# Performance work log

Measured on AMD Instinct MI355X. Metric: run time of the kernel, lower is better.

Reference implementation:

```python
import jax, jax.numpy as jnp
import numpy as np

HIDDEN, NHEAD, NLAYERS = 128, 8, 4
N, H, W = 1, 36, 192


def _layernorm(x, w, b, eps=1e-5):
    mu = x.mean(-1, keepdims=True)
    var = ((x - mu) ** 2).mean(-1, keepdims=True)
    return (x - mu) * jax.lax.rsqrt(var + eps) * w + b


def _mha_rel(q_in, k_in, v_in, in_w, in_b, out_w, out_b, pos_sel, attn_mask):
    # q_in/k_in/v_in: [w, bsz, C]; pos_sel: [w, w, C] (already gathered by pos_indexes)
    w, bsz, C = q_in.shape
    hd = C // NHEAD
    scale = float(hd) ** -0.5
    wq, wk, wv = in_w[:C], in_w[C:2 * C], in_w[2 * C:]
    bq, bk, bv = in_b[:C], in_b[C:2 * C], in_b[2 * C:]
    q = (q_in @ wq.T + bq) * scale
    k = k_in @ wk.T + bk
    v = v_in @ wv.T + bv
    q_r = (pos_sel @ wq.T + bq) * scale            # [w,w,C]
    k_r = pos_sel @ wk.T + bk                       # [w,w,C]
    q = q.reshape(w, bsz, NHEAD, hd)
    k = k.reshape(w, bsz, NHEAD, hd)
    v = v.reshape(w, bsz, NHEAD, hd)
    q_r = q_r.reshape(w, w, NHEAD, hd)
    k_r = k_r.reshape(w, w, NHEAD, hd)
    # content-content + content-pos + pos-content -> [bsz, heads, w, w]
    attn = (jnp.einsum('wnec,vnec->newv', q, k)
            + jnp.einsum('wnec,wvec->newv', q, k_r)
            + jnp.einsum('vnec,wvec->newv', k, q_r))
    if attn_mask is not None:
        attn = attn + attn_mask[None, None]
    raw = attn
    a = jax.nn.softmax(attn, axis=-1)
    vo = jnp.einsum('newv,vnec->wnec', a, v).reshape(w, bsz, C)
    vo = vo @ out_w.T + out_b
    return vo, raw.sum(axis=1)  # raw summed over heads, [bsz,w,w]


def setup_inputs():
    key = jax.random.key(0)
    ks = jax.random.split(key, 8)
    C, L = HIDDEN, NLAYERS
    s = 0.02
    rn = lambda k, shape, sc: jax.random.normal(k, shape, dtype=jnp.float32) * sc
    return dict(
        feat_left=rn(ks[0], (N, C, H, W), 1.0),
        feat_right=rn(ks[1], (N, C, H, W), 1.0),
        pos_enc=rn(ks[2], (2 * W - 1, C), 1.0),
        sa_in_w=rn(ks[3], (L, 3 * C, C), s),
        sa_in_b=jnp.zeros((L, 3 * C), jnp.float32),
        sa_out_w=rn(ks[4], (L, C, C), s),
        sa_out_b=jnp.zeros((L, C), jnp.float32),
        sa_ln_w=jnp.ones((L, C), jnp.float32),
        sa_ln_b=jnp.zeros((L, C), jnp.float32),
        ca_in_w=rn(ks[5], (L, 3 * C, C), s),
        ca_in_b=jnp.zeros((L, 3 * C), jnp.float32),
        ca_out_w=rn(ks[6], (L, C, C), s),
        ca_out_b=jnp.zeros((L, C), jnp.float32),
        ca_ln1_w=jnp.ones((L, C), jnp.float32),
        ca_ln1_b=jnp.zeros((L, C), jnp.float32),
        ca_ln2_w=jnp.ones((L, C), jnp.float32),
        ca_ln2_b=jnp.zeros((L, C), jnp.float32),
    )


def reference(feat_left, feat_right, pos_enc,
              sa_in_w, sa_in_b, sa_out_w, sa_out_b, sa_ln_w, sa_ln_b,
              ca_in_w, ca_in_b, ca_out_w, ca_out_b,
              ca_ln1_w, ca_ln1_b, ca_ln2_w, ca_ln2_b):
    n, C, h, w = feat_left.shape
    hn = h * n
    # [N,C,H,W] -> [W,HN,C]
    fl = jnp.transpose(feat_left, (3, 2, 0, 1)).reshape(w, hn, C)
    fr = jnp.transpose(feat_right, (3, 2, 0, 1)).reshape(w, hn, C)
    # relative position indexes: (w-1..0) col + (0..w-1) row, flattened
    idx = (np.arange(w - 1, -1, -1)[:, None] + np.arange(w)[None, :]).reshape(-1)
    pos_sel = pos_enc[idx].reshape(w, w, C)             # for left-query attention
    pos_sel_flip = pos_enc[::-1][idx].reshape(w, w, C)  # flipped pos for right-query
    causal_mask = jnp.triu(jnp.full((w, w), -jnp.inf, dtype=jnp.float32), k=1)

    feat = jnp.concatenate([fl, fr], axis=1)  # [W, 2HN, C]
    raw_last = None
    for i in range(NLAYERS):
        # ---- self attention on concatenated tokens ----
        f2 = _layernorm(feat, sa_ln_w[i], sa_ln_b[i])
        vo, _ = _mha_rel(f2, f2, f2, sa_in_w[i], sa_in_b[i], sa_out_w[i], sa_out_b[i],
                         pos_sel, None)
        feat = feat + vo
        # ---- cross attention (shared weights for both directions) ----
        left, right = feat[:, :hn], feat[:, hn:]
        l2 = _layernorm(left, ca_ln1_w[i], ca_ln1_b[i])
        r2 = _layernorm(right, ca_ln1_w[i], ca_ln1_b[i])
        vo, _ = _mha_rel(r2, l2, l2, ca_in_w[i], ca_in_b[i], ca_out_w[i], ca_out_b[i],
                         pos_sel_flip, None)
        right = right + vo
        mask = causal_mask if i == NLAYERS - 1 else None
        r2b = _layernorm(right, ca_ln2_w[i], ca_ln2_b[i])
        vo, raw = _mha_rel(l2, r2b, r2b, ca_in_w[i], ca_in_b[i], ca_out_w[i], ca_out_b[i],
                           pos_sel, mask)
        left = left + vo
        feat = jnp.concatenate([left, right], axis=1)
        raw_last = raw
    # raw_last: [HN, W, W] -> [N, H, W, W]
    attn_weight = raw_last.reshape(h, n, w, w).transpose(1, 0, 2, 3)
    return attn_weight, feat
```

## Files before the change

### kernel.cpp

```cpp
#include <hip/hip_runtime.h>
#include <cmath>

#define W 192
#define CC 128
#define BSA 72
#define BCA 36
#define TSA (W*BSA)
#define TCA (W*BCA)
#define CH 32
#define SLD 200

__global__ __launch_bounds__(256) void pack_feat_k(const float* __restrict__ fl,
                                                   const float* __restrict__ fr,
                                                   float* __restrict__ feat) {
  __shared__ float tile[32][33];
  int b = blockIdx.z;
  const float* src = (b < BCA) ? fl : fr;
  int h = (b < BCA) ? b : b - BCA;
  int w0 = blockIdx.x * 32, c0 = blockIdx.y * 32;
  int tx = threadIdx.x & 31, ty = threadIdx.x >> 5;
#pragma unroll
  for (int rr = 0; rr < 4; ++rr) {
    int c = ty + rr * 8;
    tile[c][tx] = src[((c0 + c) * BCA + h) * W + w0 + tx];
  }
  __syncthreads();
#pragma unroll
  for (int rr = 0; rr < 4; ++rr) {
    int wl = ty + rr * 8;
    feat[(((w0 + wl) * BSA) + b) * CC + c0 + tx] = tile[tx][wl];
  }
}

template<int TM, bool LNA>
__device__ __forceinline__ void gemm_core(
    const float* __restrict__ A, int lda, int aob, int aooff,
    const float* __restrict__ lnw, const float* __restrict__ lnb,
    const float* __restrict__ Bw, int ldb,
    const float* __restrict__ bias,
    float* __restrict__ C, float* __restrict__ Cb, int ldc,
    int M, int N, int noff, int scale_abs, int accum, int ob, int ooff) {
  constexpr int MR = TM / 16;
  constexpr int AS = TM + 4;
  __shared__ float AsT[32 * AS];
  __shared__ float BsT[32 * 132];
  int tid = threadIdx.x;
  int ty = tid >> 4, tx = tid & 15;
  int t0 = blockIdx.x * TM, n0 = blockIdx.y * 128;
  int row_l = tid >> 3, qk7 = tid & 7;
  float acc[MR][8] = {};

  float4 va[TM / 32][4];
  if constexpr (LNA) {
    float4 gv[4], bvv[4];
#pragma unroll
    for (int c4 = 0; c4 < 4; ++c4) {
      gv[c4]  = *reinterpret_cast<const float4*>(lnw + c4 * 32 + qk7 * 4);
      bvv[c4] = *reinterpret_cast<const float4*>(lnb + c4 * 32 + qk7 * 4);
    }
#pragma unroll
    for (int p = 0; p < TM / 32; ++p) {
      int ar = t0 + row_l + p * 32;
      if (ar >= M) ar = M - 1;
      int sr = (ar / aob) * BSA + (ar % aob) + aooff;
      const float* arow = A + (long)sr * lda;
      float sum = 0.f, sq = 0.f;
#pragma unroll
      for (int c4 = 0; c4 < 4; ++c4) {
        va[p][c4] = *reinterpret_cast<const float4*>(arow + c4 * 32 + qk7 * 4);
        sum += va[p][c4].x + va[p][c4].y + va[p][c4].z + va[p][c4].w;
        sq += va[p][c4].x * va[p][c4].x + va[p][c4].y * va[p][c4].y
            + va[p][c4].z * va[p][c4].z + va[p][c4].w * va[p][c4].w;
      }
      sum += __shfl_xor(sum, 1); sum += __shfl_xor(sum, 2); sum += __shfl_xor(sum, 4);
      sq  += __shfl_xor(sq, 1);  sq  += __shfl_xor(sq, 2);  sq  += __shfl_xor(sq, 4);
      float mu = sum * (1.f / 128.f);
      float var = sq * (1.f / 128.f) - mu * mu;
      float rstd = 1.0f / sqrtf(var + 1e-5f);
#pragma unroll
      for (int c4 = 0; c4 < 4; ++c4) {
        va[p][c4].x = (va[p][c4].x - mu) * rstd * gv[c4].x + bvv[c4].x;
        va[p][c4].y = (va[p][c4].y - mu) * rstd * gv[c4].y + bvv[c4].y;
        va[p][c4].z = (va[p][c4].z - mu) * rstd * gv[c4].z + bvv[c4].z;
        va[p][c4].w = (va[p][c4].w - mu) * rstd * gv[c4].w + bvv[c4].w;
      }
    }
  }

  for (int kcc = 0; kcc < 4; ++kcc) {
    int kc = kcc * 32;
#pragma unroll
    for (int p = 0; p < TM / 32; ++p) {
      int row = row_l + p * 32;
      float4 av;
      if constexpr (LNA) {
        av = va[p][kcc];
      } else {
        int arow = t0 + row;
        av = make_float4(0.f, 0.f, 0.f, 0.f);
        if (arow < M) av = *reinterpret_cast<const float4*>(A + (long)arow * lda + kc + qk7 * 4);
      }
      AsT[(qk7 * 4 + 0) * AS + row] = av.x;
      AsT[(qk7 * 4 + 1) * AS + row] = av.y;
      AsT[(qk7 * 4 + 2) * AS + row] = av.z;
      AsT[(qk7 * 4 + 3) * AS + row] = av.w;
    }
#pragma unroll
    for (int p = 0; p < 4; ++p) {
      int id = tid + p * 256;
      int row = id >> 3, qk = id & 7;
      int brow = n0 + row;
      float4 bv = make_float4(0.f, 0.f, 0.f, 0.f);
      if (brow < N) bv = *reinterpret_cast<const float4*>(Bw + (long)brow * ldb + kc + qk * 4);
      BsT[(qk * 4 + 0) * 132 + row] = bv.x;
      BsT[(qk * 4 + 1) * 132 + row] = bv.y;
      BsT[(qk * 4 + 2) * 132 + row] = bv.z;
      BsT[(qk * 4 + 3) * 132 + row] = bv.w;
    }
    __syncthreads();
#pragma unroll
    for (int k = 0; k < 32; ++k) {
      float a[MR];
      if constexpr (MR == 2) {
        float2 a0 = *reinterpret_cast<const float2*>(&AsT[k * AS + ty * 2]);
        a[0] = a0.x; a[1] = a0.y;
      } else if constexpr (MR == 4) {
        float4 a0 = *reinterpret_cast<const float4*>(&AsT[k * AS + ty * 4]);
        a[0] = a0.x; a[1] = a0.y; a[2] = a0.z; a[3] = a0.w;
      } else {
        float4 a0 = *reinterpret_cast<const float4*>(&AsT[k * AS + ty * 8]);
        float4 a1 = *reinterpret_cast<const float4*>(&AsT[k * AS + ty * 8 + 4]);
        a[0] = a0.x; a[1] = a0.y; a[2] = a0.z; a[3] = a0.w;
        a[4] = a1.x; a[5] = a1.y; a[6] = a1.z; a[7] = a1.w;
      }
      float4 b0 = *reinterpret_cast<const float4*>(&BsT[k * 132 + tx * 8]);
      float4 b1 = *reinterpret_cast<const float4*>(&BsT[k * 132 + tx * 8 + 4]);
      float bb[8] = {b0.x, b0.y, b0.z, b0.w, b1.x, b1.y, b1.z, b1.w};
#pragma unroll
      for (int i2 = 0; i2 < MR; ++i2)
#pragma unroll
        for (int j2 = 0; j2 < 8; ++j2)
          acc[i2][j2] += a[i2] * bb[j2];
    }
    __syncthreads();
  }
#pragma unroll
  for (int i2 = 0; i2 < MR; ++i2) {
    int t = t0 + ty * MR + i2;
    if (t >= M) continue;
    int orow = ob ? ((t / ob) * BSA + (t % ob) + ooff) : t;
    float* crow = C + (long)orow * ldc + noff;
    float* crow2 = Cb ? Cb + (long)orow * ldc + noff : nullptr;
#pragma unroll
    for (int j2 = 0; j2 < 8; ++j2) {
      int n = n0 + tx * 8 + j2;
      if (n >= N) continue;
      float val = acc[i2][j2] + (bias ? bias[n] : 0.f);
      if (noff + n < scale_abs) val *= 0.25f;
      if (accum) val += crow[n];
      crow[n] = val;
      if (crow2) crow2[n] = val;
    }
  }
}

template<int TM>
__global__ __launch_bounds__(256) void gemm_g(
    const float* __restrict__ A, int lda, long abatch,
    const float* __restrict__ Bw, int ldb, long bbatch,
    const float* __restrict__ bias, int bzoff,
    float* __restrict__ C, float* __restrict__ Cb, int ldc, long cbatch,
    int M, int N, int noff, int nzoff, int scale_abs, int accum, int ob, int ooff) {
  int z = blockIdx.z;
  gemm_core<TM, false>(A + z * abatch, lda, 0, 0, nullptr, nullptr,
                       Bw + z * bbatch, ldb,
                       bias ? bias + z * bzoff : nullptr,
                       C + z * cbatch, Cb, ldc, M, N, noff + z * nzoff,
                       scale_abs, accum, ob, ooff);
}

__global__ __launch_bounds__(256) void sa_qkv_k(
    const float* __restrict__ feat,
    const float* __restrict__ lnw, const float* __restrict__ lnb,
    const float* __restrict__ w3, const float* __restrict__ b3,
    float* __restrict__ out) {
  int z = blockIdx.z;
  gemm_core<64, true>(feat, 128, 72, 0, lnw, lnb,
                      w3 + z * 16384, 128, b3 + z * 128,
                      out, nullptr, 384, TSA, 128, z * 128, 128, 0, 0, 0);
}

__global__ __launch_bounds__(256) void ca_qkv_k(
    const float* __restrict__ feat,
    const float* __restrict__ lnwA, const float* __restrict__ lnbA, int ooffA,
    const float* __restrict__ lnwB, const float* __restrict__ lnbB, int ooffB,
    const float* __restrict__ w3, const float* __restrict__ b3,
    float* __restrict__ out) {
  int z = blockIdx.z;
  const float* lw = (z == 0) ? lnwA : lnwB;
  const float* lb = (z == 0) ? lnbA : lnbB;
  int aoo = (z == 0) ? ooffA : ooffB;
  gemm_core<32, true>(feat, 128, 36, aoo, lw, lb,
                      w3 + z * 16384, 128, b3 + z * 128,
                      out, nullptr, 384, TCA, 128, z * 128, 128, 0, 0, 0);
}

__global__ __launch_bounds__(256) void pos_all_k(
    const float* __restrict__ pos,
    const float* __restrict__ saw, const float* __restrict__ sab,
    const float* __restrict__ caw, const float* __restrict__ cab,
    float* __restrict__ out) {
  int z = blockIdx.z;
  int layer = z >> 2, kind = z & 3;
  const float* w = ((kind < 2) ? saw : caw) + layer * 49152 + (kind & 1) * 16384;
  const float* b = ((kind < 2) ? sab : cab) + layer * 384 + (kind & 1) * 128;
  int sc = (kind & 1) ? 0 : 128;
  gemm_core<32, false>(pos, 128, 0, 0, nullptr, nullptr, w, 128, b,
                       out + (long)z * 49152, nullptr, 128,
                       383, 128, 0, sc, 0, 0, 0);
}

__global__ __launch_bounds__(384) void attn_k(const float* __restrict__ qkv,
                                              const float* __restrict__ qpos,
                                              const float* __restrict__ kpos,
                                              float* __restrict__ vo,
                                              int B, int flip, int domask) {
  __shared__ float q_s[CH * 20];
  __shared__ float v_s[192 * 17];
  __shared__ float u_s[2 * 223 * 20];
  __shared__ float part[384];
  __shared__ float red_m[CH], red_il[CH];
  float* kp_s = u_s;
  float* qp_s = u_s + 223 * 20;
  float* S = u_s;

  int t = threadIdx.x;
  int col = (t >= 192) ? t - 192 : t;
  int rbase = (t >= 192) ? 16 : 0;
  int b = blockIdx.z, e = blockIdx.y, w0 = blockIdx.x * CH;

  for (int idx = t; idx < 192 * 4; idx += 384) {
    int row = idx >> 2, q4 = idx & 3;
    float4 kv = *reinterpret_cast<const float4*>(qkv + ((long)row * B + b) * 384 + 128 + e * 16 + q4 * 4);
    v_s[row * 17 + q4 * 4 + 0] = kv.x; v_s[row * 17 + q4 * 4 + 1] = kv.y;
    v_s[row * 17 + q4 * 4 + 2] = kv.z; v_s[row * 17 + q4 * 4 + 3] = kv.w;
  }
  __syncthreads();
  float kr[16];
#pragma unroll
  for (int d = 0; d < 16; ++d) kr[d] = v_s[col * 17 + d];
  __syncthreads();
  for (int idx = t; idx < 192 * 4; idx += 384) {
    int row = idx >> 2, q4 = idx & 3;
    float4 vv = *reinterpret_cast<const float4*>(qkv + ((long)row * B + b) * 384 + 256 + e * 16 + q4 * 4);
    v_s[row * 17 + q4 * 4 + 0] = vv.x; v_s[row * 17 + q4 * 4 + 1] = vv.y;
    v_s[row * 17 + q4 * 4 + 2] = vv.z; v_s[row * 17 + q4 * 4 + 3] = vv.w;
  }
  if (t < CH * 4) {
    int row = t >> 2, q4 = t & 3;
    float4 qv = *reinterpret_cast<const float4*>(qkv + ((long)(w0 + row) * B + b) * 384 + e * 16 + q4 * 4);
    *reinterpret_cast<float4*>(q_s + row * 20 + q4 * 4) = qv;
  }
  int base = flip ? w0 : (191 - (w0 + CH - 1));
  for (int idx = t; idx < 223 * 4; idx += 384) {
    int row = idx >> 2, q4 = idx & 3;
    int gidx = base + row;
    float4 kpv = make_float4(0.f, 0.f, 0.f, 0.f), qpv = kpv;
    if (gidx >= 0 && gidx < 383) {
      kpv = *reinterpret_cast<const float4*>(kpos + (long)gidx * 128 + e * 16 + q4 * 4);
      qpv = *reinterpret_cast<const float4*>(qpos + (long)gidx * 128 + e * 16 + q4 * 4);
    }
    *reinterpret_cast<float4*>(kp_s + row * 20 + q4 * 4) = kpv;
    *reinterpret_cast<float4*>(qp_s + row * 20 + q4 * 4) = qpv;
  }
  __syncthreads();

  float s[16];
#pragma unroll
  for (int rr = 0; rr < 16; ++rr) {
    int r = rbase + rr;
    int j = flip ? (191 + r - col) : (CH - 1 - r + col);
    const float4* kp4 = reinterpret_cast<const float4*>(kp_s + j * 20);
    const float4* qp4 = reinterpret_cast<const float4*>(qp_s + j * 20);
    const float4* qq4 = reinterpret_cast<const float4*>(q_s + r * 20);
    float acc = 0.f;
#pragma unroll
    for (int d4 = 0; d4 < 4; ++d4) {
      float4 kp = kp4[d4], qp = qp4[d4], qq = qq4[d4];
      acc += qq.x * (kr[d4 * 4 + 0] + kp.x) + kr[d4 * 4 + 0] * qp.x;
      acc += qq.y * (kr[d4 * 4 + 1] + kp.y) + kr[d4 * 4 + 1] * qp.y;
      acc += qq.z * (kr[d4 * 4 + 2] + kp.z) + kr[d4 * 4 + 2] * qp.z;
      acc += qq.w * (kr[d4 * 4 + 3] + kp.w) + kr[d4 * 4 + 3] * qp.w;
    }
    s[rr] = (domask && col > w0 + r) ? -INFINITY : acc;
  }
  __syncthreads();

#pragma unroll
  for (int rr = 0; rr < 16; ++rr) S[(rbase + rr) * SLD + col] = s[rr];
  __syncthreads();

  int r12 = t / 12, tr = t - r12 * 12;
  {
    float mloc = -INFINITY;
#pragma unroll
    for (int i = 0; i < 16; ++i) mloc = fmaxf(mloc, S[r12 * SLD + tr + 12 * i]);
    part[r12 * 12 + tr] = mloc;
  }
  __syncthreads();
  if (t < CH) {
    float m = part[t * 12];
#pragma unroll
    for (int i = 1; i < 12; ++i) m = fmaxf(m, part[t * 12 + i]);
    red_m[t] = m;
  }
  __syncthreads();
  {
    float m = red_m[r12];
    float lloc = 0.f;
#pragma unroll
    for (int i = 0; i < 16; ++i) {
      int a = r12 * SLD + tr + 12 * i;
      float p = __expf(S[a] - m);
      S[a] = p;
      lloc += p;
    }
    part[r12 * 12 + tr] = lloc;
  }
  __syncthreads();
  if (t < CH) {
    float l = 0.f;
#pragma unroll
    for (int i = 0; i < 12; ++i) l += part[t * 12 + i];
    red_il[t] = 1.0f / l;
  }
  __syncthreads();

  int d = t & 15, g = t >> 4;
  int r0 = g, r1 = g + 24;
  float a0 = 0.f, a1 = 0.f;
#pragma unroll 8
  for (int v4 = 0; v4 < 48; ++v4) {
    float4 s0 = *reinterpret_cast<const float4*>(S + r0 * SLD + v4 * 4);
    float va = v_s[(v4 * 4 + 0) * 17 + d];
    float vb = v_s[(v4 * 4 + 1) * 17 + d];
    float vc = v_s[(v4 * 4 + 2) * 17 + d];
    float vd = v_s[(v4 * 4 + 3) * 17 + d];
    a0 += s0.x * va + s0.y * vb + s0.z * vc + s0.w * vd;
    if (g < 8) {
      float4 s1 = *reinterpret_cast<const float4*>(S + r1 * SLD + v4 * 4);
      a1 += s1.x * va + s1.y * vb + s1.z * vc + s1.w * vd;
    }
  }
  vo[((long)(w0 + r0) * B + b) * 128 + e * 16 + d] = a0 * red_il[r0];
  if (g < 8)
    vo[((long)(w0 + r1) * B + b) * 128 + e * 16 + d] = a1 * red_il[r1];
}

__global__ __launch_bounds__(256) void gather_k(const float* __restrict__ D,
                                                const float* __restrict__ E,
                                                float* __restrict__ out) {
  __shared__ float E_s[192][33];
  int b = blockIdx.y, w0 = blockIdx.x * 32;
  for (int idx = threadIdx.x; idx < 192 * 32; idx += 256) {
    int v = idx >> 5, j = idx & 31;
    int u = 160 + v - w0 + j;
    E_s[v][j] = (u >= 0 && u < 192) ? E[((long)v * BCA + b) * 192 + u] : 0.f;
  }
  __syncthreads();
  int lane = threadIdx.x & 63, wl = threadIdx.x >> 6;
#pragma unroll
  for (int i = 0; i < 8; ++i) {
    int w = w0 + wl * 8 + i;
    int j = w0 + 31 - w;
#pragma unroll
    for (int kv = 0; kv < 3; ++kv) {
      int v = lane + kv * 64;
      long o = ((long)b * W + w) * W + v;
      if (v > w) {
        out[o] = -1e30f;
      } else {
        out[o] = out[o] + D[((long)w * BCA + b) * 192 + 191 + v - w] + E_s[v][j];
      }
    }
  }
}

extern "C" void kernel_launch(void* const* d_in, const int* in_sizes, int n_in,
                              void* d_out, int out_size, void* d_ws, size_t ws_size,
                              hipStream_t stream) {
  (void)in_sizes; (void)n_in; (void)out_size; (void)ws_size;
  const float* feat_left  = (const float*)d_in[0];
  const float* feat_right = (const float*)d_in[1];
  const float* pos_enc    = (const float*)d_in[2];
  const float* sa_in_w    = (const float*)d_in[3];
  const float* sa_in_b    = (const float*)d_in[4];
  const float* sa_out_w   = (const float*)d_in[5];
  const float* sa_out_b   = (const float*)d_in[6];
  const float* sa_ln_w    = (const float*)d_in[7];
  const float* sa_ln_b    = (const float*)d_in[8];
  const float* ca_in_w    = (const float*)d_in[9];
  const float* ca_in_b    = (const float*)d_in[10];
  const float* ca_out_w   = (const float*)d_in[11];
  const float* ca_out_b   = (const float*)d_in[12];
  const float* ca_ln1_w   = (const float*)d_in[13];
  const float* ca_ln1_b   = (const float*)d_in[14];
  const float* ca_ln2_w   = (const float*)d_in[15];
  const float* ca_ln2_b   = (const float*)d_in[16];

  float* ws   = (float*)d_ws;
  float* feat = ws;
  float* qkv  = feat + 1769472;
  float* vo   = qkv + 5308416;
  float* posA = vo + 1769472;
  float* Dbuf = qkv + 2654208;
  float* Ebuf = Dbuf + 1327104;

  float* raw_out  = (float*)d_out;
  float* feat_out = raw_out + 1327104;

  pack_feat_k<<<dim3(6, 4, 72), 256, 0, stream>>>(feat_left, feat_right, feat);
  pos_all_k<<<dim3(12, 1, 16), 256, 0, stream>>>(pos_enc, sa_in_w, sa_in_b, ca_in_w, ca_in_b, posA);

  for (int i = 0; i < 4; ++i) {
    const float* inw  = sa_in_w + i * 49152;
    const float* inb  = sa_in_b + i * 384;
    const float* outw = sa_out_w + i * 16384;
    const float* outb = sa_out_b + i * 128;
    const float* saQ = posA + (long)(i * 4 + 0) * 49152;
    const float* saK = posA + (long)(i * 4 + 1) * 49152;
    const float* caQ = posA + (long)(i * 4 + 2) * 49152;
    const float* caK = posA + (long)(i * 4 + 3) * 49152;
    const float* ln1w = ca_ln1_w + i * 128, *ln1b = ca_ln1_b + i * 128;
    const float* ln2w = ca_ln2_w + i * 128, *ln2b = ca_ln2_b + i * 128;
    float* fo = (i == 3) ? feat_out : nullptr;

    sa_qkv_k<<<dim3(216, 1, 3), 256, 0, stream>>>(feat, sa_ln_w + i * 128, sa_ln_b + i * 128, inw, inb, qkv);
    attn_k<<<dim3(6, 8, 72), 384, 0, stream>>>(qkv, saQ, saK, vo, 72, 0, 0);
    gemm_g<32><<<dim3(432, 1, 1), 256, 0, stream>>>(vo, 128, 0, outw, 128, 0, outb, 0,
                                                    feat, nullptr, 128, 0, TSA, 128, 0, 0, 0, 1, 0, 0);

    const float* cinw  = ca_in_w + i * 49152;
    const float* cinb  = ca_in_b + i * 384;
    const float* coutw = ca_out_w + i * 16384;
    const float* coutb = ca_out_b + i * 128;
    ca_qkv_k<<<dim3(216, 1, 3), 256, 0, stream>>>(feat, ln1w, ln1b, 36, ln1w, ln1b, 0, cinw, cinb, qkv);
    attn_k<<<dim3(6, 8, 36), 384, 0, stream>>>(qkv, caQ, caK, vo, 36, 1, 0);
    gemm_g<32><<<dim3(216, 1, 1), 256, 0, stream>>>(vo, 128, 0, coutw, 128, 0, coutb, 0,
                                                    feat, fo, 128, 0, TCA, 128, 0, 0, 0, 1, 36, 36);
    ca_qkv_k<<<dim3(216, 1, 3), 256, 0, stream>>>(feat, ln1w, ln1b, 0, ln2w, ln2b, 36, cinw, cinb, qkv);
    attn_k<<<dim3(6, 8, 36), 384, 0, stream>>>(qkv, caQ, caK, vo, 36, 0, (i == 3) ? 1 : 0);
    if (i == 3) {
      gemm_g<32><<<dim3(216, 2, 2), 256, 0, stream>>>(qkv, 384, 128, caK, 128, -49152, nullptr, 0,
                                                      Dbuf, nullptr, 192, 1327104, TCA, 192, 0, 0, 0, 0, 0, 0);
      gemm_g<32><<<dim3(6, 2, 36), 256, 0, stream>>>(qkv, 13824, 384, qkv + 128, 13824, 384, nullptr, 0,
                                                     raw_out, nullptr, 192, 36864, 192, 192, 0, 0, 0, 0, 0, 0);
      gather_k<<<dim3(6, 36), 256, 0, stream>>>(Dbuf, Ebuf, raw_out);
    }
    gemm_g<32><<<dim3(216, 1, 1), 256, 0, stream>>>(vo, 128, 0, coutw, 128, 0, coutb, 0,
                                                    feat, fo, 128, 0, TCA, 128, 0, 0, 0, 1, 36, 0);
  }
}
```

Measured before the change: 1.626 ms.

## Enlarge GEMM row tiles, add streaming layernorm mode, vectorize softmax passes

Doubles the M-tile of the QKV and out-projection GEMMs (64→128 for self-attn QKV, 32→64 for cross QKV and the SA out-proj) and halves their grid sizes, so each block reuses the loaded weight tile across more rows. A new layernorm mode computes only per-row mean/rstd up front and re-reads and normalizes A per K-chunk, which avoids holding the whole normalized row in registers at the larger tile. The attention softmax now reads each thread's contiguous 16-score slice as float4s held in registers, instead of strided scalar shared-memory accesses. Larger tiles raise register and LDS pressure and leave fewer blocks to fill the CUs.

```diff
diff --git a/kernel.cpp b/kernel.cpp
--- a/kernel.cpp
+++ b/kernel.cpp
@@ -32,7 +32,7 @@
   }
 }
 
-template<int TM, bool LNA>
+template<int TM, int LNMODE>
 __device__ __forceinline__ void gemm_core(
     const float* __restrict__ A, int lda, int aob, int aooff,
     const float* __restrict__ lnw, const float* __restrict__ lnb,
@@ -50,8 +50,9 @@
   int row_l = tid >> 3, qk7 = tid & 7;
   float acc[MR][8] = {};
 
-  float4 va[TM / 32][4];
-  if constexpr (LNA) {
+  float4 va[(LNMODE == 1) ? TM / 32 : 1][4];
+  float mu2[TM / 32], rs2[TM / 32];
+  if constexpr (LNMODE == 1) {
     float4 gv[4], bvv[4];
 #pragma unroll
     for (int c4 = 0; c4 < 4; ++c4) {
@@ -85,6 +86,27 @@
         va[p][c4].w = (va[p][c4].w - mu) * rstd * gv[c4].w + bvv[c4].w;
       }
     }
+  } else if constexpr (LNMODE == 2) {
+#pragma unroll
+    for (int p = 0; p < TM / 32; ++p) {
+      int ar = t0 + row_l + p * 32;
+      if (ar >= M) ar = M - 1;
+      int sr = (ar / aob) * BSA + (ar % aob) + aooff;
+      const float* arow = A + (long)sr * lda;
+      float sum = 0.f, sq = 0.f;
+#pragma unroll
+      for (int c4 = 0; c4 < 4; ++c4) {
+        float4 v = *reinterpret_cast<const float4*>(arow + c4 * 32 + qk7 * 4);
+        sum += v.x + v.y + v.z + v.w;
+        sq += v.x * v.x + v.y * v.y + v.z * v.z + v.w * v.w;
+      }
+      sum += __shfl_xor(sum, 1); sum += __shfl_xor(sum, 2); sum += __shfl_xor(sum, 4);
+      sq  += __shfl_xor(sq, 1);  sq  += __shfl_xor(sq, 2);  sq  += __shfl_xor(sq, 4);
+      float mu = sum * (1.f / 128.f);
+      float var = sq * (1.f / 128.f) - mu * mu;
+      mu2[p] = mu;
+      rs2[p] = 1.0f / sqrtf(var + 1e-5f);
+    }
   }
 
   for (int kcc = 0; kcc < 4; ++kcc) {
@@ -93,8 +115,19 @@
     for (int p = 0; p < TM / 32; ++p) {
       int row = row_l + p * 32;
       float4 av;
-      if constexpr (LNA) {
+      if constexpr (LNMODE == 1) {
         av = va[p][kcc];
+      } else if constexpr (LNMODE == 2) {
+        int ar = t0 + row;
+        if (ar >= M) ar = M - 1;
+        int sr = (ar / aob) * BSA + (ar % aob) + aooff;
+        av = *reinterpret_cast<const float4*>(A + (long)sr * lda + kc + qk7 * 4);
+        float4 gq = *reinterpret_cast<const float4*>(lnw + kc + qk7 * 4);
+        float4 bq = *reinterpret_cast<const float4*>(lnb + kc + qk7 * 4);
+        av.x = (av.x - mu2[p]) * rs2[p] * gq.x + bq.x;
+        av.y = (av.y - mu2[p]) * rs2[p] * gq.y + bq.y;
+        av.z = (av.z - mu2[p]) * rs2[p] * gq.z + bq.z;
+        av.w = (av.w - mu2[p]) * rs2[p] * gq.w + bq.w;
       } else {
         int arow = t0 + row;
         av = make_float4(0.f, 0.f, 0.f, 0.f);
@@ -172,11 +205,11 @@
     float* __restrict__ C, float* __restrict__ Cb, int ldc, long cbatch,
     int M, int N, int noff, int nzoff, int scale_abs, int accum, int ob, int ooff) {
   int z = blockIdx.z;
-  gemm_core<TM, false>(A + z * abatch, lda, 0, 0, nullptr, nullptr,
-                       Bw + z * bbatch, ldb,
-                       bias ? bias + z * bzoff : nullptr,
-                       C + z * cbatch, Cb, ldc, M, N, noff + z * nzoff,
-                       scale_abs, accum, ob, ooff);
+  gemm_core<TM, 0>(A + z * abatch, lda, 1, 0, nullptr, nullptr,
+                   Bw + z * bbatch, ldb,
+                   bias ? bias + z * bzoff : nullptr,
+                   C + z * cbatch, Cb, ldc, M, N, noff + z * nzoff,
+                   scale_abs, accum, ob, ooff);
 }
 
 __global__ __launch_bounds__(256) void sa_qkv_k(
@@ -185,9 +218,9 @@
     const float* __restrict__ w3, const float* __restrict__ b3,
     float* __restrict__ out) {
   int z = blockIdx.z;
-  gemm_core<64, true>(feat, 128, 72, 0, lnw, lnb,
-                      w3 + z * 16384, 128, b3 + z * 128,
-                      out, nullptr, 384, TSA, 128, z * 128, 128, 0, 0, 0);
+  gemm_core<128, 2>(feat, 128, 72, 0, lnw, lnb,
+                    w3 + z * 16384, 128, b3 + z * 128,
+                    out, nullptr, 384, TSA, 128, z * 128, 128, 0, 0, 0);
 }
 
 __global__ __launch_bounds__(256) void ca_qkv_k(
@@ -200,9 +233,9 @@
   const float* lw = (z == 0) ? lnwA : lnwB;
   const float* lb = (z == 0) ? lnbA : lnbB;
   int aoo = (z == 0) ? ooffA : ooffB;
-  gemm_core<32, true>(feat, 128, 36, aoo, lw, lb,
-                      w3 + z * 16384, 128, b3 + z * 128,
-                      out, nullptr, 384, TCA, 128, z * 128, 128, 0, 0, 0);
+  gemm_core<64, 1>(feat, 128, 36, aoo, lw, lb,
+                   w3 + z * 16384, 128, b3 + z * 128,
+                   out, nullptr, 384, TCA, 128, z * 128, 128, 0, 0, 0);
 }
 
 __global__ __launch_bounds__(256) void pos_all_k(
@@ -215,9 +248,9 @@
   const float* w = ((kind < 2) ? saw : caw) + layer * 49152 + (kind & 1) * 16384;
   const float* b = ((kind < 2) ? sab : cab) + layer * 384 + (kind & 1) * 128;
   int sc = (kind & 1) ? 0 : 128;
-  gemm_core<32, false>(pos, 128, 0, 0, nullptr, nullptr, w, 128, b,
-                       out + (long)z * 49152, nullptr, 128,
-                       383, 128, 0, sc, 0, 0, 0);
+  gemm_core<32, 0>(pos, 128, 1, 0, nullptr, nullptr, w, 128, b,
+                   out + (long)z * 49152, nullptr, 128,
+                   383, 128, 0, sc, 0, 0, 0);
 }
 
 __global__ __launch_bounds__(384) void attn_k(const float* __restrict__ qkv,
@@ -301,11 +334,15 @@
   __syncthreads();
 
   int r12 = t / 12, tr = t - r12 * 12;
+  float4 xx[4];
   {
     float mloc = -INFINITY;
 #pragma unroll
-    for (int i = 0; i < 16; ++i) mloc = fmaxf(mloc, S[r12 * SLD + tr + 12 * i]);
-    part[r12 * 12 + tr] = mloc;
+    for (int q = 0; q < 4; ++q) {
+      xx[q] = *reinterpret_cast<const float4*>(S + r12 * SLD + tr * 16 + q * 4);
+      mloc = fmaxf(mloc, fmaxf(fmaxf(xx[q].x, xx[q].y), fmaxf(xx[q].z, xx[q].w)));
+    }
+    part[t] = mloc;
   }
   __syncthreads();
   if (t < CH) {
@@ -319,13 +356,15 @@
     float m = red_m[r12];
     float lloc = 0.f;
 #pragma unroll
-    for (int i = 0; i < 16; ++i) {
-      int a = r12 * SLD + tr + 12 * i;
-      float p = __expf(S[a] - m);
-      S[a] = p;
-      lloc += p;
-    }
-    part[r12 * 12 + tr] = lloc;
+    for (int q = 0; q < 4; ++q) {
+      xx[q].x = __expf(xx[q].x - m);
+      xx[q].y = __expf(xx[q].y - m);
+      xx[q].z = __expf(xx[q].z - m);
+      xx[q].w = __expf(xx[q].w - m);
+      lloc += xx[q].x + xx[q].y + xx[q].z + xx[q].w;
+      *reinterpret_cast<float4*>(S + r12 * SLD + tr * 16 + q * 4) = xx[q];
+    }
+    part[t] = lloc;
   }
   __syncthreads();
   if (t < CH) {
@@ -435,23 +474,23 @@
     const float* ln2w = ca_ln2_w + i * 128, *ln2b = ca_ln2_b + i * 128;
     float* fo = (i == 3) ? feat_out : nullptr;
 
-    sa_qkv_k<<<dim3(216, 1, 3), 256, 0, stream>>>(feat, sa_ln_w + i * 128, sa_ln_b + i * 128, inw, inb, qkv);
+    sa_qkv_k<<<dim3(108, 1, 3), 256, 0, stream>>>(feat, sa_ln_w + i * 128, sa_ln_b + i * 128, inw, inb, qkv);
     attn_k<<<dim3(6, 8, 72), 384, 0, stream>>>(qkv, saQ, saK, vo, 72, 0, 0);
-    gemm_g<32><<<dim3(432, 1, 1), 256, 0, stream>>>(vo, 128, 0, outw, 128, 0, outb, 0,
+    gemm_g<64><<<dim3(216, 1, 1), 256, 0, stream>>>(vo, 128, 0, outw, 128, 0, outb, 0,
                                                     feat, nullptr, 128, 0, TSA, 128, 0, 0, 0, 1, 0, 0);
 
     const float* cinw  = ca_in_w + i * 49152;
     const float* cinb  = ca_in_b + i * 384;
     const float* coutw = ca_out_w + i * 16384;
     const float* coutb = ca_out_b + i * 128;
-    ca_qkv_k<<<dim3(216, 1, 3), 256, 0, stream>>>(feat, ln1w, ln1b, 36, ln1w, ln1b, 0, cinw, cinb, qkv);
+    ca_qkv_k<<<dim3(108, 1, 3), 256, 0, stream>>>(feat, ln1w, ln1b, 36, ln1w, ln1b, 0, cinw, cinb, qkv);
     attn_k<<<dim3(6, 8, 36), 384, 0, stream>>>(qkv, caQ, caK, vo, 36, 1, 0);
     gemm_g<32><<<dim3(216, 1, 1), 256, 0, stream>>>(vo, 128, 0, coutw, 128, 0, coutb, 0,
                                                     feat, fo, 128, 0, TCA, 128, 0, 0, 0, 1, 36, 36);
-    ca_qkv_k<<<dim3(216, 1, 3), 256, 0, stream>>>(feat, ln1w, ln1b, 0, ln2w, ln2b, 36, cinw, cinb, qkv);
+    ca_qkv_k<<<dim3(108, 1, 3), 256, 0, stream>>>(feat, ln1w, ln1b, 0, ln2w, ln2b, 36, cinw, cinb, qkv);
     attn_k<<<dim3(6, 8, 36), 384, 0, stream>>>(qkv, caQ, caK, vo, 36, 0, (i == 3) ? 1 : 0);
     if (i == 3) {
-      gemm_g<32><<<dim3(216, 2, 2), 256, 0, stream>>>(qkv, 384, 128, caK, 128, -49152, nullptr, 0,
+      gemm_g<64><<<dim3(108, 2, 2), 256, 0, stream>>>(qkv, 384, 128, caK, 128, -49152, nullptr, 0,
                                                       Dbuf, nullptr, 192, 1327104, TCA, 192, 0, 0, 0, 0, 0, 0);
       gemm_g<32><<<dim3(6, 2, 36), 256, 0, stream>>>(qkv, 13824, 384, qkv + 128, 13824, 384, nullptr, 0,
                                                      raw_out, nullptr, 192, 36864, 192, 192, 0, 0, 0, 0, 0, 0);
```

Result: slower. 1.707 ms (+5.0%).
